# Kernel tuning notes

Hardware: AMD Instinct MI355X
Metric: run time of the kernel (lower is better)

The kernel has to match this reference:

```python
import jax, jax.numpy as jnp
import numpy as np

HIDDEN = 2048
INTER = 8192
COMPRESSION = 128.9

def _n_ctrl(out_size, in_size):
    return max(16, int(out_size * in_size / COMPRESSION))

def _catmull_rom_grid(n_ctrl, n_samples):
    # static (numpy, float64) sampling grid over [0, n_ctrl-1] to avoid fp32 precision loss
    t = np.linspace(0.0, n_ctrl - 1.0, n_samples, dtype=np.float64)
    i = np.clip(np.floor(t).astype(np.int64), 0, n_ctrl - 2)
    f = (t - i).astype(np.float32)
    idx = np.stack([np.clip(i + k, 0, n_ctrl - 1) for k in (-1, 0, 1, 2)], axis=0)  # [4, N]
    return jnp.asarray(idx.astype(np.int32)), jnp.asarray(f)

def spline_reconstruct(control_points, out_size, in_size):
    """Cubic (Catmull-Rom, order-3) interpolation of 1D control points to a dense [out,in] weight."""
    n = out_size * in_size
    idx, f = _catmull_rom_grid(control_points.shape[0], n)
    p0, p1, p2, p3 = control_points[idx[0]], control_points[idx[1]], control_points[idx[2]], control_points[idx[3]]
    f2 = f * f
    f3 = f2 * f
    w = 0.5 * (2.0 * p1 + (p2 - p0) * f
               + (2.0 * p0 - 5.0 * p1 + 4.0 * p2 - p3) * f2
               + (3.0 * p1 - p0 - 3.0 * p2 + p3) * f3)
    return w.reshape(out_size, in_size)

def setup_inputs() -> dict:
    key = jax.random.key(0)
    k0, k1, k2, k3 = jax.random.split(key, 4)
    hidden_states = jax.random.normal(k0, (4, 2048, HIDDEN), dtype=jnp.float32)
    gate_cp = jax.random.normal(k1, (_n_ctrl(INTER, HIDDEN),), dtype=jnp.float32) * 0.02
    up_cp = jax.random.normal(k2, (_n_ctrl(INTER, HIDDEN),), dtype=jnp.float32) * 0.02
    down_cp = jax.random.normal(k3, (_n_ctrl(HIDDEN, INTER),), dtype=jnp.float32) * 0.02
    return {"hidden_states": hidden_states, "gate_cp": gate_cp, "up_cp": up_cp, "down_cp": down_cp}

def reference(hidden_states, gate_cp, up_cp, down_cp):
    gate_w = spline_reconstruct(gate_cp, INTER, HIDDEN)   # [I, H]
    up_w = spline_reconstruct(up_cp, INTER, HIDDEN)       # [I, H]
    down_w = spline_reconstruct(down_cp, HIDDEN, INTER)   # [H, I]
    gate = jnp.einsum('bsh,ih->bsi', hidden_states, gate_w)
    up = jnp.einsum('bsh,ih->bsi', hidden_states, up_w)
    inter = jax.nn.silu(gate) * up
    return jnp.einsum('bsi,hi->bsh', inter, down_w)
```

## Files before the change

### kernel.cpp

```cpp
#include <hip/hip_runtime.h>
#include <hip/hip_bf16.h>
#include <math.h>

using bf16 = __hip_bfloat16;
typedef __bf16 bf16x8 __attribute__((ext_vector_type(8)));
typedef float  f32x4  __attribute__((ext_vector_type(4)));

#define BK 64

__global__ void spline_recon8_kernel(const float* __restrict__ cp,
                                     bf16* __restrict__ w,
                                     int n8, int n_ctrl, double step) {
    int k8 = blockIdx.x * blockDim.x + threadIdx.x;
    if (k8 >= n8) return;
    long long kbase = (long long)k8 * 8;
    bf16x8 o;
#pragma unroll
    for (int u = 0; u < 8; ++u) {
        double t = (double)(kbase + u) * step;
        int i = (int)t;
        if (i > n_ctrl - 2) i = n_ctrl - 2;
        float f = (float)(t - (double)i);
        float p0 = cp[i > 0 ? i - 1 : 0];
        float p1 = cp[i];
        float p2 = cp[i + 1];
        float p3 = cp[(i + 2) <= (n_ctrl - 1) ? (i + 2) : (n_ctrl - 1)];
        float f2 = f * f;
        float f3 = f2 * f;
        float v = 0.5f * (2.0f * p1
                          + (p2 - p0) * f
                          + (2.0f * p0 - 5.0f * p1 + 4.0f * p2 - p3) * f2
                          + (3.0f * p1 - p0 - 3.0f * p2 + p3) * f3);
        o[u] = (__bf16)v;
    }
    *reinterpret_cast<bf16x8*>(w + kbase) = o;
}

__global__ void cvt_f32_bf16_8_kernel(const float4* __restrict__ x,
                                      bf16* __restrict__ y, int n8) {
    int k = blockIdx.x * blockDim.x + threadIdx.x;
    if (k >= n8) return;
    float4 a = x[2 * k];
    float4 b = x[2 * k + 1];
    bf16x8 o;
    o[0] = (__bf16)a.x; o[1] = (__bf16)a.y; o[2] = (__bf16)a.z; o[3] = (__bf16)a.w;
    o[4] = (__bf16)b.x; o[5] = (__bf16)b.y; o[6] = (__bf16)b.z; o[7] = (__bf16)b.w;
    *reinterpret_cast<bf16x8*>(y + (long long)k * 8) = o;
}

__device__ __forceinline__ void async_load16(const bf16* g, bf16* l) {
    __builtin_amdgcn_global_load_lds(
        (const __attribute__((address_space(1))) void*)g,
        (__attribute__((address_space(3))) void*)l,
        16, 0, 0);
}

__global__ __launch_bounds__(512, 4) void fused_gate_up_kernel(
    const bf16* __restrict__ A,
    const bf16* __restrict__ Bg,
    const bf16* __restrict__ Bu,
    bf16* __restrict__ C,
    int M, int N, int K) {
    __shared__ __align__(16) bf16 smem[3 * 128 * BK];
    bf16* As  = smem;
    bf16* Bgs = smem + 128 * BK;
    bf16* Bus = smem + 2 * 128 * BK;

    const int tid  = threadIdx.x;
    const int lane = tid & 63;
    const int wave = tid >> 6;
    const int wq   = wave & 3;
    const int wm   = (wq >> 1) * 64;
    const int wn   = (wq & 1) * 64;
    const bool is_gate = wave < 4;

    const long long brow = (long long)blockIdx.y * 128;
    const long long bcol = (long long)blockIdx.x * 128;

    const int srow = tid >> 3;
    const int skb  = ((tid & 7) ^ (srow & 7)) * 8;
    const bf16* ga0 = A  + (brow + srow) * (long long)K + skb;
    const bf16* ga1 = A  + (brow + srow + 64) * (long long)K + skb;
    const bf16* gg0 = Bg + (bcol + srow) * (long long)K + skb;
    const bf16* gg1 = Bg + (bcol + srow + 64) * (long long)K + skb;
    const bf16* gu0 = Bu + (bcol + srow) * (long long)K + skb;
    const bf16* gu1 = Bu + (bcol + srow + 64) * (long long)K + skb;
    bf16* la0 = As  + tid * 8;
    bf16* la1 = As  + 4096 + tid * 8;
    bf16* lg0 = Bgs + tid * 8;
    bf16* lg1 = Bgs + 4096 + tid * 8;
    bf16* lu0 = Bus + tid * 8;
    bf16* lu1 = Bus + 4096 + tid * 8;

    const bf16* Bsel = is_gate ? Bgs : Bus;
    const int fm = wm + (lane & 15);
    const int fn = wn + (lane & 15);
    const int qk = lane >> 4;

    f32x4 acc[4][4] = {};

    for (int k0 = 0; k0 < K; k0 += BK) {
        async_load16(ga0, la0); ga0 += BK;
        async_load16(ga1, la1); ga1 += BK;
        async_load16(gg0, lg0); gg0 += BK;
        async_load16(gg1, lg1); gg1 += BK;
        async_load16(gu0, lu0); gu0 += BK;
        async_load16(gu1, lu1); gu1 += BK;
        __syncthreads();

#pragma unroll
        for (int h = 0; h < 2; ++h) {
            bf16x8 afr[4], bfr[4];
            const int hc = (h << 2) | qk;
            const int ccA = (hc ^ (fm & 7)) * 8;
            const int ccB = (hc ^ (fn & 7)) * 8;
#pragma unroll
            for (int i = 0; i < 4; ++i)
                afr[i] = *reinterpret_cast<const bf16x8*>(
                    &As[(fm + i * 16) * BK + ccA]);
#pragma unroll
            for (int j = 0; j < 4; ++j)
                bfr[j] = *reinterpret_cast<const bf16x8*>(
                    &Bsel[(fn + j * 16) * BK + ccB]);
#pragma unroll
            for (int i = 0; i < 4; ++i)
#pragma unroll
                for (int j = 0; j < 4; ++j)
                    acc[i][j] = __builtin_amdgcn_mfma_f32_16x16x32_bf16(
                        afr[i], bfr[j], acc[i][j], 0, 0, 0);
        }
        __syncthreads();
    }

    bf16* Epi = smem;
    if (is_gate) {
#pragma unroll
        for (int i = 0; i < 4; ++i)
#pragma unroll
            for (int j = 0; j < 4; ++j)
#pragma unroll
                for (int r = 0; r < 4; ++r) {
                    int row = wm + i * 16 + (lane >> 4) * 4 + r;
                    int col = wn + j * 16 + (lane & 15);
                    float v = acc[i][j][r];
                    float s = v / (1.0f + expf(-v));
                    Epi[row * 128 + col] = __float2bfloat16(s);
                }
    }
    __syncthreads();
    if (!is_gate) {
#pragma unroll
        for (int i = 0; i < 4; ++i)
#pragma unroll
            for (int j = 0; j < 4; ++j)
#pragma unroll
                for (int r = 0; r < 4; ++r) {
                    int row = wm + i * 16 + (lane >> 4) * 4 + r;
                    int col = wn + j * 16 + (lane & 15);
                    float s = __bfloat162float(Epi[row * 128 + col]);
                    float v = s * acc[i][j][r];
                    C[(brow + row) * (long long)N + bcol + col] = __float2bfloat16(v);
                }
    }
}

__global__ __launch_bounds__(512, 2) void gemm_down5_kernel(
    const bf16* __restrict__ A,
    const bf16* __restrict__ B,
    float* __restrict__ C,
    int M, int N, int K) {
    __shared__ __align__(16) bf16 smem[2 * 3 * 128 * BK];
    bf16* As0 = smem;
    bf16* Bs0 = smem + 128 * BK;
    bf16* As1 = smem + 3 * 128 * BK;
    bf16* Bs1 = smem + 4 * 128 * BK;

    const int tid  = threadIdx.x;
    const int lane = tid & 63;
    const int wave = tid >> 6;
    const int wm   = (wave >> 2) * 64;
    const int wn   = (wave & 3) * 64;

    const int b = blockIdx.x;
    const long long brow = (long long)((b & 7) * 8 + (b >> 6)) * 128;
    const long long bcol = (long long)((b >> 3) & 7) * 256;

    const int srow = tid >> 3;
    const int skb  = ((tid & 7) ^ (srow & 7)) * 8;
    const bf16* ga0 = A + (brow + srow) * (long long)K + skb;
    const bf16* ga1 = A + (brow + srow + 64) * (long long)K + skb;
    const bf16* gb0 = B + (bcol + srow) * (long long)K + skb;
    const bf16* gb1 = B + (bcol + srow + 64) * (long long)K + skb;
    const bf16* gb2 = B + (bcol + srow + 128) * (long long)K + skb;
    const bf16* gb3 = B + (bcol + srow + 192) * (long long)K + skb;

    const int fm = wm + (lane & 15);
    const int fn = wn + (lane & 15);
    const int qk = lane >> 4;

    f32x4 acc[4][4] = {};

#define STAGE_DOWN(dA, dB, t)                                              \
    do {                                                                   \
        long long off = (long long)(t) * BK;                               \
        async_load16(ga0 + off, (dA) + tid * 8);                           \
        async_load16(ga1 + off, (dA) + 4096 + tid * 8);                    \
        async_load16(gb0 + off, (dB) + tid * 8);                           \
        async_load16(gb1 + off, (dB) + 4096 + tid * 8);                    \
        async_load16(gb2 + off, (dB) + 8192 + tid * 8);                    \
        async_load16(gb3 + off, (dB) + 12288 + tid * 8);                   \
    } while (0)

#define COMPUTE_DOWN(sA, sB)                                               \
    do {                                                                   \
        _Pragma("unroll")                                                  \
        for (int h = 0; h < 2; ++h) {                                      \
            bf16x8 afr[4], bfr[4];                                         \
            const int hc = (h << 2) | qk;                                  \
            const int ccA = (hc ^ (fm & 7)) * 8;                           \
            const int ccB = (hc ^ (fn & 7)) * 8;                           \
            _Pragma("unroll")                                              \
            for (int i = 0; i < 4; ++i)                                    \
                afr[i] = *reinterpret_cast<const bf16x8*>(                 \
                    &(sA)[(fm + i * 16) * BK + ccA]);                      \
            _Pragma("unroll")                                              \
            for (int j = 0; j < 4; ++j)                                    \
                bfr[j] = *reinterpret_cast<const bf16x8*>(                 \
                    &(sB)[(fn + j * 16) * BK + ccB]);                      \
            _Pragma("unroll")                                              \
            for (int i = 0; i < 4; ++i)                                    \
                _Pragma("unroll")                                          \
                for (int j = 0; j < 4; ++j)                                \
                    acc[i][j] = __builtin_amdgcn_mfma_f32_16x16x32_bf16(   \
                        afr[i], bfr[j], acc[i][j], 0, 0, 0);               \
        }                                                                  \
    } while (0)

    const int nt = K / BK;

    STAGE_DOWN(As0, Bs0, 0);
    __syncthreads();

    for (int t = 0; t < nt; t += 2) {
        if (t + 1 < nt) STAGE_DOWN(As1, Bs1, t + 1);
        COMPUTE_DOWN(As0, Bs0);
        __syncthreads();
        if (t + 2 < nt) STAGE_DOWN(As0, Bs0, t + 2);
        COMPUTE_DOWN(As1, Bs1);
        __syncthreads();
    }
#undef STAGE_DOWN
#undef COMPUTE_DOWN

#pragma unroll
    for (int i = 0; i < 4; ++i)
#pragma unroll
        for (int j = 0; j < 4; ++j)
#pragma unroll
            for (int r = 0; r < 4; ++r) {
                long long row = brow + wm + i * 16 + qk * 4 + r;
                long long col = bcol + wn + j * 16 + (lane & 15);
                C[row * N + col] = acc[i][j][r];
            }
}

extern "C" void kernel_launch(void* const* d_in, const int* in_sizes, int n_in,
                              void* d_out, int out_size, void* d_ws, size_t ws_size,
                              hipStream_t stream) {
    const float* hs  = (const float*)d_in[0];
    const float* gcp = (const float*)d_in[1];
    const float* ucp = (const float*)d_in[2];
    const float* dcp = (const float*)d_in[3];

    const int M = 8192;
    const int H = 2048;
    const int I = 8192;
    const int NW = H * I;
    const int n_ctrl_g = in_sizes[1];
    const int n_ctrl_u = in_sizes[2];
    const int n_ctrl_d = in_sizes[3];

    bf16* Xb    = (bf16*)d_ws;
    bf16* Wg    = Xb + (size_t)M * H;
    bf16* Wu    = Wg + (size_t)NW;
    bf16* Wd    = Wu + (size_t)NW;
    bf16* inter = Wd + (size_t)NW;

    const int nX8 = (M * H) / 8;
    cvt_f32_bf16_8_kernel<<<(nX8 + 255) / 256, 256, 0, stream>>>(
        (const float4*)hs, Xb, nX8);

    double step_g = (double)(n_ctrl_g - 1) / (double)(NW - 1);
    double step_u = (double)(n_ctrl_u - 1) / (double)(NW - 1);
    double step_d = (double)(n_ctrl_d - 1) / (double)(NW - 1);
    const int n8 = NW / 8;
    spline_recon8_kernel<<<(n8 + 255) / 256, 256, 0, stream>>>(gcp, Wg, n8, n_ctrl_g, step_g);
    spline_recon8_kernel<<<(n8 + 255) / 256, 256, 0, stream>>>(ucp, Wu, n8, n_ctrl_u, step_u);
    spline_recon8_kernel<<<(n8 + 255) / 256, 256, 0, stream>>>(dcp, Wd, n8, n_ctrl_d, step_d);

    fused_gate_up_kernel<<<dim3(I / 128, M / 128), 512, 0, stream>>>(
        Xb, Wg, Wu, inter, M, I, H);

    gemm_down5_kernel<<<512, 512, 0, stream>>>(
        inter, Wd, (float*)d_out, M, H, I);
}
```

Before: 938.6 us.

## Prefetch two tiles ahead in down GEMM with partial vmcnt waits

The down-projection GEMM now issues async global-to-LDS loads two K tiles ahead. It waits only until the older tile's loads have landed (vmcnt(6)) and uses raw s_barrier in place of __syncthreads, so the next tile's loads stay in flight while the current tile is computed. This is meant to hide global memory latency behind the MFMA work. The hand-counted vmcnt value is fragile: if STAGE_DOWN issues a different number of loads per thread, or the compiler adds other memory ops, it could read stale LDS data.

```diff
diff --git a/kernel.cpp b/kernel.cpp
--- a/kernel.cpp
+++ b/kernel.cpp
@@ -55,6 +55,12 @@
         16, 0, 0);
 }
 
+__device__ __forceinline__ void raw_barrier() {
+    asm volatile("" ::: "memory");
+    __builtin_amdgcn_s_barrier();
+    asm volatile("" ::: "memory");
+}
+
 __global__ __launch_bounds__(512, 4) void fused_gate_up_kernel(
     const bf16* __restrict__ A,
     const bf16* __restrict__ Bg,
@@ -164,7 +170,7 @@
     }
 }
 
-__global__ __launch_bounds__(512, 2) void gemm_down5_kernel(
+__global__ __launch_bounds__(512, 2) void gemm_down6_kernel(
     const bf16* __restrict__ A,
     const bf16* __restrict__ B,
     float* __restrict__ C,
@@ -236,21 +242,36 @@
         }                                                                  \
     } while (0)
 
+#define WAIT_VM6() asm volatile("s_waitcnt vmcnt(6)" ::: "memory")
+#define WAIT_VM0() asm volatile("s_waitcnt vmcnt(0)" ::: "memory")
+
     const int nt = K / BK;
 
     STAGE_DOWN(As0, Bs0, 0);
-    __syncthreads();
-
-    for (int t = 0; t < nt; t += 2) {
-        if (t + 1 < nt) STAGE_DOWN(As1, Bs1, t + 1);
+    STAGE_DOWN(As1, Bs1, 1);
+    WAIT_VM6();
+    raw_barrier();
+
+    for (int t = 0; t + 2 < nt; t += 2) {
         COMPUTE_DOWN(As0, Bs0);
-        __syncthreads();
-        if (t + 2 < nt) STAGE_DOWN(As0, Bs0, t + 2);
+        raw_barrier();
+        STAGE_DOWN(As0, Bs0, t + 2);
+        WAIT_VM6();
+        raw_barrier();
         COMPUTE_DOWN(As1, Bs1);
-        __syncthreads();
-    }
+        raw_barrier();
+        STAGE_DOWN(As1, Bs1, t + 3);
+        WAIT_VM6();
+        raw_barrier();
+    }
+    COMPUTE_DOWN(As0, Bs0);
+    WAIT_VM0();
+    raw_barrier();
+    COMPUTE_DOWN(As1, Bs1);
 #undef STAGE_DOWN
 #undef COMPUTE_DOWN
+#undef WAIT_VM6
+#undef WAIT_VM0
 
 #pragma unroll
     for (int i = 0; i < 4; ++i)
@@ -301,6 +322,6 @@
     fused_gate_up_kernel<<<dim3(I / 128, M / 128), 512, 0, stream>>>(
         Xb, Wg, Wu, inter, M, I, H);
 
-    gemm_down5_kernel<<<512, 512, 0, stream>>>(
+    gemm_down6_kernel<<<512, 512, 0, stream>>>(
         inter, Wd, (float*)d_out, M, H, I);
 }
```

After: 890.7 us. -5.1%, faster.
